# Performance work log

Hardware: AMD Instinct MI355X
Metric: run time of the kernel (lower is better)

Reference implementation:

```python
import jax, jax.numpy as jnp
import numpy as np

S, B, I, H, L = 512, 64, 512, 512, 2
EPS = 1e-5


def setup_inputs() -> dict:
    key = jax.random.key(0)
    ks = jax.random.split(key, 8)
    gain = float(np.sqrt(1.0 / H))
    u = lambda k, shp: jax.random.uniform(k, shp, jnp.float32, -gain, gain)
    return {
        "inputs": jax.random.normal(ks[0], (S, B, I), jnp.float32),
        "h0": jnp.zeros((L, B, H), jnp.float32),
        "c0": jnp.zeros((L, B, H), jnp.float32),
        "wx0": u(ks[1], (I, 4 * H)),
        "wx1": u(ks[2], (H, 4 * H)),
        "wh0": u(ks[3], (H, 4 * H)),
        "wh1": u(ks[4], (H, 4 * H)),
        "bias": u(ks[5], (L, 4 * H)),
        "ln_gamma": jnp.ones((L, 4, H), jnp.float32),
        "ln_beta": jnp.zeros((L, 4, H), jnp.float32),
    }


def _layer(x, h, c, wx, wh, b, gamma, beta):
    # Precompute the input projection as one big GEMM: [S,B,4H]
    xg = jnp.einsum('sbi,ig->sbg', x, wx) + b

    def cell(carry, xg_t):
        h, c = carry
        gate = xg_t + h @ wh                      # [B, 4H]
        g = gate.reshape(B, 4, H)
        mu = jnp.mean(g, axis=-1, keepdims=True)
        var = jnp.var(g, axis=-1, keepdims=True)
        g = (g - mu) * jax.lax.rsqrt(var + EPS) * gamma + beta
        i, f, o, u = g[:, 0], g[:, 1], g[:, 2], g[:, 3]
        c = jax.nn.sigmoid(f) * c + jax.nn.sigmoid(i) * jnp.tanh(u)
        h = jax.nn.sigmoid(o) * jnp.tanh(c)
        return (h, c), h

    (h, c), ys = jax.lax.scan(cell, (h, c), xg)
    return ys, h, c


def reference(inputs, h0, c0, wx0, wx1, wh0, wh1, bias, ln_gamma, ln_beta):
    x = inputs
    wxs, whs = [wx0, wx1], [wh0, wh1]
    hs, cs = [], []
    for l in range(L):
        x, h, c = _layer(x, h0[l], c0[l], wxs[l], whs[l], bias[l], ln_gamma[l], ln_beta[l])
        hs.append(h)
        cs.append(c)
    return x, jnp.stack(hs, 0), jnp.stack(cs, 0)
```

## Files before the change

kernel.cpp:

```cpp
#include <hip/hip_runtime.h>


#define NTH 256

typedef float f32x4 __attribute__((ext_vector_type(4)));

__device__ __forceinline__ float sigm(float x) { return 1.f / (1.f + __expf(-x)); }
__device__ __forceinline__ float tanh_f(float x) { return 2.f / (1.f + __expf(-2.f * x)) - 1.f; }

__device__ __forceinline__ unsigned long long pack2(float a, float b) {
  union { float f[2]; unsigned long long u; } x; x.f[0] = a; x.f[1] = b; return x.u;
}
__device__ __forceinline__ void sys_store64(unsigned long long* p, unsigned long long v) {
  __hip_atomic_store(p, v, __ATOMIC_RELAXED, __HIP_MEMORY_SCOPE_SYSTEM);
}

__device__ __forceinline__ void post(unsigned int* flag, unsigned int val) {
  __syncthreads();
  if (threadIdx.x == 0)
    __hip_atomic_store(flag, val, __ATOMIC_RELEASE, __HIP_MEMORY_SCOPE_SYSTEM);
}

__device__ __forceinline__ void waitall(const unsigned int* flags, unsigned int target) {
  long guard = 0;
  for (;;) {
    int ok = 1;
    if (threadIdx.x < 128) {
      unsigned int v = __hip_atomic_load(&flags[threadIdx.x * 32],
                                         __ATOMIC_RELAXED, __HIP_MEMORY_SCOPE_SYSTEM);
      ok = (v >= target);
    }
    if (__syncthreads_and(ok)) break;
    if (++guard > (1L << 22)) break;
  }
  __atomic_signal_fence(__ATOMIC_ACQUIRE);
}

__global__ __launch_bounds__(NTH, 1)
void lstm_pk(const float* __restrict__ inputs, const float* __restrict__ h0,
             const float* __restrict__ c0,
             const float* __restrict__ wx0, const float* __restrict__ wx1,
             const float* __restrict__ wh0, const float* __restrict__ wh1,
             const float* __restrict__ bias, const float* __restrict__ gamma_,
             const float* __restrict__ beta_,
             float* __restrict__ out,
             unsigned int* flags,
             unsigned long long* slots,
             float* __restrict__ h_state)
{
  extern __shared__ float lds[];
  float* W_lds = lds;
  float* A_lds = lds + 16384;
  float* part  = lds + 16384 + 17408;
  float* gates = part + 4352;
  float* minv  = gates + 1024;

  const int tid = threadIdx.x;
  const int wg = blockIdx.x;
  const int layer = wg >> 7;
  const int w = wg & 127;
  const int wavet = tid >> 6;
  const int lane = tid & 63;
  const int rq = lane & 15;
  const int gq = lane >> 4;
  const int srow = tid >> 2;
  const int sg = tid & 3;
  const int hc = 4 * w + sg;

  const float* Wx = layer ? wx1 : wx0;
  const float* Wh = layer ? wh1 : wh0;

  for (int i = 0; i < 16; ++i) {
    int e = tid + i * 256;
    int k = e >> 2, g = e & 3;
    const float* src = (k < 512) ? (Wx + (size_t)k * 2048)
                                 : (Wh + (size_t)(k - 512) * 2048);
    f32x4 v = *(const f32x4*)(src + g * 512 + 4 * w);
    *(f32x4*)&W_lds[k * 16 + g * 4] = v;
  }

  f32x4 biasr = *(const f32x4*)(bias + layer * 2048 + sg * 512 + 4 * w);
  float gam[4], bet[4];
#pragma unroll
  for (int g = 0; g < 4; ++g) {
    gam[g] = gamma_[layer * 2048 + g * 512 + hc];
    bet[g] = beta_[layer * 2048 + g * 512 + hc];
  }
  float c_st = c0[layer * 32768 + srow * 512 + hc];

  unsigned long long* slotL = slots + (size_t)layer * 32768;
  float* hstL = h_state + layer * 32768;
  unsigned int* fmyL = flags + layer * 4096;
  unsigned int* myflag = fmyL + w * 32;
  const unsigned int* fL0 = flags;

  const int strow = rq + 16 * wavet;

  f32x4 st[8];
  auto LOADC = [&](const float* src, int koff) {
    const float* s = src + strow * 512 + koff;
#pragma unroll
    for (int i = 0; i < 8; ++i)
      st[i] = *(const f32x4*)(s + 4 * (gq + 4 * i));
  };
  auto WRITEC = [&](int b) {
    float* dst = A_lds + b * 8704;
#pragma unroll
    for (int i = 0; i < 8; ++i) {
      int kq = gq + 4 * i;
#pragma unroll
      for (int j = 0; j < 4; ++j)
        dst[(4 * kq + j) * 68 + strow] = st[i][j];
    }
  };
  auto COMPUTEC = [&](int kW, int b, f32x4* acc) {
    const float* Ab = A_lds + b * 8704;
    const int kg = kW + wavet * 32;
#pragma unroll 8
    for (int kk = 0; kk < 32; ++kk) {
      int k = wavet * 32 + kk;
      f32x4 av = *(const f32x4*)&Ab[k * 68 + 4 * rq];
      f32x4 wv = *(const f32x4*)&W_lds[(kg + kk) * 16 + gq * 4];
      acc[0] += av[0] * wv;
      acc[1] += av[1] * wv;
      acc[2] += av[2] * wv;
      acc[3] += av[3] * wv;
    }
  };
  auto GEMM4 = [&](const float* src, int wbase, f32x4* acc) {
    LOADC(src, 0);
    WRITEC(0);
    __syncthreads();
#pragma unroll 1
    for (int i = 0; i < 4; ++i) {
      if (i < 3) LOADC(src, (i + 1) * 128);
      COMPUTEC(wbase + i * 128, i & 1, acc);
      if (i < 3) WRITEC((i + 1) & 1);
      __syncthreads();
    }
  };

  f32x4 acc_x[4];
#pragma unroll
  for (int r = 0; r < 4; ++r) acc_x[r] = (f32x4){0.f, 0.f, 0.f, 0.f};
  if (layer == 0) {
    GEMM4(inputs, 0, acc_x);
  } else {
    waitall(fL0, 2u);
    __builtin_amdgcn_fence(__ATOMIC_ACQUIRE, "agent");
    GEMM4(out, 0, acc_x);
  }

  for (int t = 0; t < 512; ++t) {
    const unsigned int t2 = 2u * (unsigned)t;
    const float* hsrc = (t == 0) ? (h0 + layer * 32768) : hstL;

    if (t) {
      waitall(fmyL, t2);
      __builtin_amdgcn_fence(__ATOMIC_ACQUIRE, "agent");
    }
    f32x4 acc_h[4];
#pragma unroll
    for (int r = 0; r < 4; ++r) acc_h[r] = (f32x4){0.f, 0.f, 0.f, 0.f};
    GEMM4(hsrc, 512, acc_h);

#pragma unroll
    for (int r = 0; r < 4; ++r)
#pragma unroll
      for (int cc = 0; cc < 4; ++cc)
        part[(wavet * 64 + 4 * rq + r) * 17 + gq * 4 + cc] = acc_h[r][cc] + acc_x[r][cc];
    __syncthreads();

    {
      f32x4 pre;
#pragma unroll
      for (int cc = 0; cc < 4; ++cc) {
        float v = biasr[cc];
        v += part[(0 * 64 + srow) * 17 + sg * 4 + cc];
        v += part[(1 * 64 + srow) * 17 + sg * 4 + cc];
        v += part[(2 * 64 + srow) * 17 + sg * 4 + cc];
        v += part[(3 * 64 + srow) * 17 + sg * 4 + cc];
        pre[cc] = v;
      }
      *(f32x4*)&gates[srow * 16 + sg * 4] = pre;
      float s = ((pre[0] + pre[1]) + pre[2]) + pre[3];
      float ss = ((pre[0] * pre[0] + pre[1] * pre[1]) + pre[2] * pre[2]) + pre[3] * pre[3];
      sys_store64(&slotL[(size_t)w * 256 + tid], pack2(s, ss));
    }
    post(myflag, t2 + 1u);

#pragma unroll
    for (int r = 0; r < 4; ++r) acc_x[r] = (f32x4){0.f, 0.f, 0.f, 0.f};
    if (t < 511) {
      if (layer == 1) {
        waitall(fL0, t2 + 4u);
        __builtin_amdgcn_fence(__ATOMIC_ACQUIRE, "agent");
      }
      const float* xn = (layer ? out : inputs) + (size_t)(t + 1) * 32768;
      GEMM4(xn, 0, acc_x);
    }

    waitall(fmyL, t2 + 1u);
    __builtin_amdgcn_fence(__ATOMIC_ACQUIRE, "agent");

    {
      float Sc[8], SSc[8];
#pragma unroll
      for (int j = 0; j < 8; ++j) { Sc[j] = 0.f; SSc[j] = 0.f; }
#pragma unroll 4
      for (int q8 = 0; q8 < 16; ++q8) {
#pragma unroll
        for (int j = 0; j < 8; ++j) {
          unsigned long long u = *(const unsigned long long*)
              &slotL[(size_t)(q8 * 8 + j) * 256 + tid];
          union { unsigned long long u; float f[2]; } x; x.u = u;
          Sc[j] += x.f[0]; SSc[j] += x.f[1];
        }
      }
      float S = ((Sc[0] + Sc[1]) + (Sc[2] + Sc[3])) + ((Sc[4] + Sc[5]) + (Sc[6] + Sc[7]));
      float SS = ((SSc[0] + SSc[1]) + (SSc[2] + SSc[3])) + ((SSc[4] + SSc[5]) + (SSc[6] + SSc[7]));
      float mu = S * (1.f / 512.f);
      float var = SS * (1.f / 512.f) - mu * mu;
      minv[tid * 2 + 0] = mu;
      minv[tid * 2 + 1] = rsqrtf(fmaxf(var, 0.f) + 1e-5f);
    }
    __syncthreads();

    {
      float gv[4];
#pragma unroll
      for (int g = 0; g < 4; ++g) {
        float pre = gates[srow * 16 + g * 4 + sg];
        gv[g] = (pre - minv[(srow * 4 + g) * 2]) * minv[(srow * 4 + g) * 2 + 1] * gam[g] + bet[g];
      }
      float ig = sigm(gv[0]);
      float fg = sigm(gv[1]);
      float og = sigm(gv[2]);
      float ug = tanh_f(gv[3]);
      c_st = fg * c_st + ig * ug;
      float hv = og * tanh_f(c_st);

      float hv2 = __shfl_down(hv, 1);
      float cv2 = __shfl_down(c_st, 1);
      if ((sg & 1) == 0) {
        unsigned long long hp = pack2(hv, hv2);
        sys_store64((unsigned long long*)&hstL[srow * 512 + hc], hp);
        sys_store64((unsigned long long*)&out[(size_t)t * 32768 + srow * 512 + hc], hp);
        if (t == 511) {
          sys_store64((unsigned long long*)&out[16777216 + layer * 32768 + srow * 512 + hc], hp);
          sys_store64((unsigned long long*)&out[16842752 + layer * 32768 + srow * 512 + hc],
                      pack2(c_st, cv2));
        }
      }
    }
    post(myflag, t2 + 2u);
  }
}

extern "C" void kernel_launch(void* const* d_in, const int* in_sizes, int n_in,
                              void* d_out, int out_size, void* d_ws, size_t ws_size,
                              hipStream_t stream) {
  const float* inputs = (const float*)d_in[0];
  const float* h0 = (const float*)d_in[1];
  const float* c0 = (const float*)d_in[2];
  const float* wx0 = (const float*)d_in[3];
  const float* wx1 = (const float*)d_in[4];
  const float* wh0 = (const float*)d_in[5];
  const float* wh1 = (const float*)d_in[6];
  const float* bias = (const float*)d_in[7];
  const float* gamma_ = (const float*)d_in[8];
  const float* beta_ = (const float*)d_in[9];
  float* out = (float*)d_out;

  char* ws = (char*)d_ws;
  unsigned int* flags = (unsigned int*)ws;
  unsigned long long* slots = (unsigned long long*)(ws + 65536);
  float* h_state = (float*)(ws + 65536 + 524288);

  const int smem_bytes = 158720;
  hipFuncSetAttribute((const void*)lstm_pk,
                      hipFuncAttributeMaxDynamicSharedMemorySize, smem_bytes);
  hipMemsetAsync(ws, 0, 65536, stream);

  hipLaunchKernelGGL(lstm_pk, dim3(256), dim3(NTH), smem_bytes, stream,
                     inputs, h0, c0, wx0, wx1, wh0, wh1, bias, gamma_, beta_,
                     out, flags, slots, h_state);
}
```

Baseline: 22.01 ms.

## Share hidden state in transposed layout, pack flags, and ring-buffer layer-0 outputs

Hidden state is now exchanged in a transposed [H,B] global buffer and consumed directly by a new register GEMM that reads it without staging through LDS. Layer 0 no longer writes its outputs to the final output tensor; it writes them into a 4-deep ring buffer that layer 1 reads. Back-pressure flags stop layer 0 from overrunning that ring. Flags are packed contiguously and polled per thread rather than through a syncthreads_and loop. This aims to cut LDS staging and synchronisation latency on the serial recurrent path, at the cost of uncoalesced 4-wide global reads per k and a tighter coupling between the two layers.

```diff
diff --git a/kernel.cpp b/kernel.cpp
--- a/kernel.cpp
+++ b/kernel.cpp
@@ -22,17 +22,14 @@
 }
 
 __device__ __forceinline__ void waitall(const unsigned int* flags, unsigned int target) {
-  long guard = 0;
-  for (;;) {
-    int ok = 1;
-    if (threadIdx.x < 128) {
-      unsigned int v = __hip_atomic_load(&flags[threadIdx.x * 32],
-                                         __ATOMIC_RELAXED, __HIP_MEMORY_SCOPE_SYSTEM);
-      ok = (v >= target);
-    }
-    if (__syncthreads_and(ok)) break;
-    if (++guard > (1L << 22)) break;
-  }
+  if (threadIdx.x < 128) {
+    long guard = 0;
+    while (__hip_atomic_load(&flags[threadIdx.x], __ATOMIC_RELAXED,
+                             __HIP_MEMORY_SCOPE_SYSTEM) < target) {
+      if (++guard > (1L << 24)) break;
+    }
+  }
+  __syncthreads();
   __atomic_signal_fence(__ATOMIC_ACQUIRE);
 }
 
@@ -46,7 +43,8 @@
              float* __restrict__ out,
              unsigned int* flags,
              unsigned long long* slots,
-             float* __restrict__ h_state)
+             float* __restrict__ h_T,
+             float* __restrict__ y0r)
 {
   extern __shared__ float lds[];
   float* W_lds = lds;
@@ -89,14 +87,35 @@
   float c_st = c0[layer * 32768 + srow * 512 + hc];
 
   unsigned long long* slotL = slots + (size_t)layer * 32768;
-  float* hstL = h_state + layer * 32768;
-  unsigned int* fmyL = flags + layer * 4096;
-  unsigned int* myflag = fmyL + w * 32;
+  float* hTL = h_T + layer * 32768;
+  unsigned int* fmyL = flags + layer * 128;
+  unsigned int* myflag = fmyL + w;
   const unsigned int* fL0 = flags;
-
+  const unsigned int* fL1 = flags + 128;
+
+  {
+    float hv = h0[layer * 32768 + srow * 512 + hc];
+    __hip_atomic_store((unsigned int*)&hTL[hc * 64 + srow],
+                       __float_as_uint(hv), __ATOMIC_RELAXED,
+                       __HIP_MEMORY_SCOPE_SYSTEM);
+  }
+  post(myflag, 1u);
+
+  auto GEMMT = [&](const float* T, int wbase, f32x4* acc) {
+    const int k0 = wavet * 128;
+#pragma unroll 8
+    for (int kk = 0; kk < 128; ++kk) {
+      int k = k0 + kk;
+      f32x4 av = *(const f32x4*)&T[(size_t)k * 64 + 4 * rq];
+      f32x4 wv = *(const f32x4*)&W_lds[(wbase + k) * 16 + gq * 4];
+      acc[0] += av[0] * wv;
+      acc[1] += av[1] * wv;
+      acc[2] += av[2] * wv;
+      acc[3] += av[3] * wv;
+    }
+  };
+  f32x4 st[8];
   const int strow = rq + 16 * wavet;
-
-  f32x4 st[8];
   auto LOADC = [&](const float* src, int koff) {
     const float* s = src + strow * 512 + koff;
 #pragma unroll
@@ -146,23 +165,20 @@
   if (layer == 0) {
     GEMM4(inputs, 0, acc_x);
   } else {
-    waitall(fL0, 2u);
+    waitall(fL0, 3u);
     __builtin_amdgcn_fence(__ATOMIC_ACQUIRE, "agent");
-    GEMM4(out, 0, acc_x);
+    GEMMT(y0r, 0, acc_x);
   }
 
   for (int t = 0; t < 512; ++t) {
     const unsigned int t2 = 2u * (unsigned)t;
-    const float* hsrc = (t == 0) ? (h0 + layer * 32768) : hstL;
-
-    if (t) {
-      waitall(fmyL, t2);
-      __builtin_amdgcn_fence(__ATOMIC_ACQUIRE, "agent");
-    }
+
+    waitall(fmyL, (t == 0) ? 1u : (t2 + 1u));
+    __builtin_amdgcn_fence(__ATOMIC_ACQUIRE, "agent");
     f32x4 acc_h[4];
 #pragma unroll
     for (int r = 0; r < 4; ++r) acc_h[r] = (f32x4){0.f, 0.f, 0.f, 0.f};
-    GEMM4(hsrc, 512, acc_h);
+    GEMMT(hTL, 512, acc_h);
 
 #pragma unroll
     for (int r = 0; r < 4; ++r)
@@ -187,20 +203,22 @@
       float ss = ((pre[0] * pre[0] + pre[1] * pre[1]) + pre[2] * pre[2]) + pre[3] * pre[3];
       sys_store64(&slotL[(size_t)w * 256 + tid], pack2(s, ss));
     }
-    post(myflag, t2 + 1u);
+    post(myflag, t2 + 2u);
 
 #pragma unroll
     for (int r = 0; r < 4; ++r) acc_x[r] = (f32x4){0.f, 0.f, 0.f, 0.f};
     if (t < 511) {
-      if (layer == 1) {
-        waitall(fL0, t2 + 4u);
+      if (layer == 0) {
+        if (t >= 5) waitall(fL1, t2 - 7u);
+        GEMM4(inputs + (size_t)(t + 1) * 32768, 0, acc_x);
+      } else {
+        waitall(fL0, t2 + 5u);
         __builtin_amdgcn_fence(__ATOMIC_ACQUIRE, "agent");
-      }
-      const float* xn = (layer ? out : inputs) + (size_t)(t + 1) * 32768;
-      GEMM4(xn, 0, acc_x);
-    }
-
-    waitall(fmyL, t2 + 1u);
+        GEMMT(y0r + (size_t)((t + 1) & 3) * 32768, 0, acc_x);
+      }
+    }
+
+    waitall(fmyL, t2 + 2u);
     __builtin_amdgcn_fence(__ATOMIC_ACQUIRE, "agent");
 
     {
@@ -240,20 +258,31 @@
       c_st = fg * c_st + ig * ug;
       float hv = og * tanh_f(c_st);
 
-      float hv2 = __shfl_down(hv, 1);
-      float cv2 = __shfl_down(c_st, 1);
-      if ((sg & 1) == 0) {
-        unsigned long long hp = pack2(hv, hv2);
-        sys_store64((unsigned long long*)&hstL[srow * 512 + hc], hp);
-        sys_store64((unsigned long long*)&out[(size_t)t * 32768 + srow * 512 + hc], hp);
-        if (t == 511) {
-          sys_store64((unsigned long long*)&out[16777216 + layer * 32768 + srow * 512 + hc], hp);
+      float hvr = __shfl_down(hv, 4);
+      if ((srow & 1) == 0) {
+        unsigned long long hp = pack2(hv, hvr);
+        sys_store64((unsigned long long*)&hTL[hc * 64 + srow], hp);
+        if (layer == 0)
+          sys_store64((unsigned long long*)&y0r[(size_t)(t & 3) * 32768 + hc * 64 + srow], hp);
+      }
+      if (layer == 1) {
+        float hv2 = __shfl_down(hv, 1);
+        if ((sg & 1) == 0)
+          sys_store64((unsigned long long*)&out[(size_t)t * 32768 + srow * 512 + hc],
+                      pack2(hv, hv2));
+      }
+      if (t == 511) {
+        float hv2 = __shfl_down(hv, 1);
+        float cv2 = __shfl_down(c_st, 1);
+        if ((sg & 1) == 0) {
+          sys_store64((unsigned long long*)&out[16777216 + layer * 32768 + srow * 512 + hc],
+                      pack2(hv, hv2));
           sys_store64((unsigned long long*)&out[16842752 + layer * 32768 + srow * 512 + hc],
                       pack2(c_st, cv2));
         }
       }
     }
-    post(myflag, t2 + 2u);
+    post(myflag, t2 + 3u);
   }
 }
 
@@ -274,15 +303,16 @@
 
   char* ws = (char*)d_ws;
   unsigned int* flags = (unsigned int*)ws;
-  unsigned long long* slots = (unsigned long long*)(ws + 65536);
-  float* h_state = (float*)(ws + 65536 + 524288);
+  unsigned long long* slots = (unsigned long long*)(ws + 4096);
+  float* h_T = (float*)(ws + 4096 + 524288);
+  float* y0r = (float*)(ws + 4096 + 524288 + 262144);
 
   const int smem_bytes = 158720;
   hipFuncSetAttribute((const void*)lstm_pk,
                       hipFuncAttributeMaxDynamicSharedMemorySize, smem_bytes);
-  hipMemsetAsync(ws, 0, 65536, stream);
+  hipMemsetAsync(ws, 0, 4096, stream);
 
   hipLaunchKernelGGL(lstm_pk, dim3(256), dim3(NTH), smem_bytes, stream,
                      inputs, h0, c0, wx0, wx1, wh0, wh1, bias, gamma_, beta_,
-                     out, flags, slots, h_state);
-}
+                     out, flags, slots, h_T, y0r);
+}
```

After: 24.25 ms. +10.2%, slower.
